# Performance work log

Hardware: AMD Instinct MI355X
Metric: run time of the kernel (lower is better)

The kernel has to match this reference:

```python
import jax, jax.numpy as jnp
import numpy as np
import math

B, T, D, DI, DFF, H = 4, 1024, 1024, 256, 4096, 16
S, N, E = 16, 256, 1024          # stat_num, token_num, exemplar_len
STAT_K, TOKEN_K = 8, 16
NEG = -1e6


def setup_inputs() -> dict:
    key = jax.random.key(0)
    ks = jax.random.split(key, 32)
    r = lambda i, shape: jax.random.normal(ks[i], shape, jnp.float32)
    w = lambda i, shape: r(i, shape) * 0.02
    return dict(
        x=r(0, (B, T, D)),
        stat_enc=r(1, (B * S, N, D)),
        exemplar_enc=r(2, (B, E, D)),
        stat_feature=r(3, (B, S, D)),
        intent_embed=r(4, (B, 1, DI)),
        Wq1=w(5, (D, D)), Wk1=w(6, (D, D)), Wv1=w(7, (D, D)), Wo1=w(8, (D, D)),
        Wq_stat=w(9, (D + DI, D)), Wq_token=w(10, (D + DI, D)),
        Wk_stat=w(11, (D, D)), Wk_token=w(12, (D, D)),
        Wv_sel=w(13, (D, D)), Wo_sel=w(14, (D, D)),
        Wq2=w(15, (D + DI, D)), Wk2=w(16, (D, D)), Wv2=w(17, (D, D)), Wo2=w(18, (D, D)),
        Wg=w(19, (2 * D, 1)),
        W1=w(20, (D, DFF)), b1=jnp.zeros((DFF,), jnp.float32),
        W2=w(21, (DFF, D)), b2=jnp.zeros((D,), jnp.float32),
        g1=jnp.ones((D,), jnp.float32), be1=jnp.zeros((D,), jnp.float32),
        g2=jnp.ones((D,), jnp.float32), be2=jnp.zeros((D,), jnp.float32),
        g3=jnp.ones((D,), jnp.float32), be3=jnp.zeros((D,), jnp.float32),
        stat_valid_len=jax.random.randint(ks[22], (B,), 1, S + 1),
        example_valid_len=jax.random.randint(ks[23], (B,), 1, E + 1),
    )


def _ln(x, g, b):
    m = x.mean(-1, keepdims=True)
    v = ((x - m) ** 2).mean(-1, keepdims=True)
    return (x - m) / jnp.sqrt(v + 1e-5) * g + b


def _mha(q, k, v, valid, Wq, Wk, Wv, Wo):
    Bq, Tq, _ = q.shape
    Sk = k.shape[1]
    sp = lambda z: z.reshape(Bq, z.shape[1], H, -1).transpose(0, 2, 1, 3)  # B,H,L,dh
    qh, kh, vh = sp(q @ Wq), sp(k @ Wk), sp(v @ Wv)
    dh = qh.shape[-1]
    sc = jnp.einsum('bhtd,bhsd->bhts', qh, kh) / math.sqrt(dh)
    vl = valid[:, None, None, None] if valid.ndim == 1 else valid[:, None, :, None]
    sc = jnp.where(jnp.arange(Sk)[None, None, None, :] < vl, sc, NEG)
    w = jax.nn.softmax(sc, axis=-1)
    out = jnp.einsum('bhts,bhsd->bhtd', w, vh).transpose(0, 2, 1, 3).reshape(Bq, Tq, -1)
    return out @ Wo


def _scatter_topk(scores, k):
    # keep top-k per row, everything else -> NEG (matches torch topk+scatter)
    shp = scores.shape
    flat = scores.reshape(-1, shp[-1])
    vals, idx = jax.lax.top_k(flat, k)
    out = jnp.full_like(flat, NEG).at[jnp.arange(flat.shape[0])[:, None], idx].set(vals)
    return out.reshape(shp)


def reference(x, stat_enc, exemplar_enc, stat_feature, intent_embed,
              Wq1, Wk1, Wv1, Wo1,
              Wq_stat, Wq_token, Wk_stat, Wk_token, Wv_sel, Wo_sel,
              Wq2, Wk2, Wv2, Wo2, Wg,
              W1, b1, W2, b2,
              g1, be1, g2, be2, g3, be3,
              stat_valid_len, example_valid_len):
    # masked self-attention (training mode -> causal valid lens)
    dec_valid = jnp.broadcast_to(jnp.arange(1, T + 1)[None, :], (B, T))
    x2 = _mha(x, x, x, dec_valid, Wq1, Wk1, Wv1, Wo1)
    y = _ln(x + x2, g1, be1)
    yi = jnp.concatenate([y, jnp.broadcast_to(intent_embed, (B, T, DI))], axis=-1)

    # selective hierarchical top-k attention
    qs = yi @ Wq_stat                      # [B,T,D]
    qt = yi @ Wq_token                     # [B,T,D]
    ks = stat_feature @ Wk_stat            # [B,S,D]
    kt = (stat_enc @ Wk_token).reshape(B, S, N, D)
    vv = (stat_enc @ Wv_sel).reshape(B, S, N, D)
    scale = math.sqrt(D)
    ssc = jnp.einsum('btd,bsd->bts', qs, ks) / scale
    ssc = jnp.where(jnp.arange(S)[None, None, :] < stat_valid_len[:, None, None], ssc, NEG)
    sw = jax.nn.softmax(_scatter_topk(ssc, min(S - 1, STAT_K)), axis=-1)   # [B,T,S]
    tsc = jnp.einsum('btd,bsnd->btsn', qt, kt) / scale                      # [B,T,S,N]
    tw = jax.nn.softmax(_scatter_topk(tsc, min(N - 1, TOKEN_K)), axis=-1)
    comb = sw[..., None] * tw                                               # [B,T,S,N]
    y2s = jnp.einsum('btsn,bsnd->btd', comb, vv) @ Wo_sel

    # exemplar cross-attention
    y2e = _mha(yi, exemplar_enc, exemplar_enc, example_valid_len, Wq2, Wk2, Wv2, Wo2)

    gate = jax.nn.sigmoid(jnp.concatenate([y2s, y2e], axis=-1) @ Wg)
    y2 = gate * y2s + (1.0 - gate) * y2e
    z = _ln(y + 2.0 * y2, g2, be2)
    ffn = jax.nn.relu(z @ W1 + b1) @ W2 + b2
    return _ln(z + ffn, g3, be3)
```

## Files before the change

kernel.cpp:

```cpp
#include <hip/hip_runtime.h>

typedef unsigned short u16;
typedef short s16x8 __attribute__((ext_vector_type(8)));
typedef u16 u16x4 __attribute__((ext_vector_type(4)));
typedef float f32x4 __attribute__((ext_vector_type(4)));

#define T_N   1024
#define NEGV  -1e6f
#define MB    (1L << 20)

__device__ __forceinline__ u16 f2bf(float f) {
    unsigned u = __float_as_uint(f);
    u += 0x7fffu + ((u >> 16) & 1u);
    return (u16)(u >> 16);
}
__device__ __forceinline__ float bf2f(u16 h) {
    return __uint_as_float(((unsigned)h) << 16);
}
__device__ __forceinline__ f32x4 mfma16(s16x8 a, s16x8 b, f32x4 c) {
    return __builtin_amdgcn_mfma_f32_16x16x32_bf16(a, b, c, 0, 0, 0);
}
__device__ __forceinline__ void gll16(const u16* g, u16* l) {
    __builtin_amdgcn_global_load_lds((const __attribute__((address_space(1))) void*)g,
                                     (__attribute__((address_space(3))) void*)l, 16, 0, 0);
}
__device__ __forceinline__ int swzf(int row) {
    return ((row >> 1) & 3) | ((row & 1) << 2);
}
__device__ __forceinline__ int swzc(int col, int row) {
    return (((col >> 3) ^ swzf(row)) << 3) | (col & 7);
}

struct P6 { const float* s[6]; u16* d[6]; };

__global__ __launch_bounds__(256) void transpose_cast_batch(P6 pp, int K, int N) {
    const float* __restrict__ src = pp.s[blockIdx.z];
    u16* __restrict__ dst = pp.d[blockIdx.z];
    __shared__ float tile[32][33];
    int nb = blockIdx.x * 32, kb = blockIdx.y * 32;
    int tx = threadIdx.x & 31, ty = threadIdx.x >> 5;
    #pragma unroll
    for (int i = 0; i < 4; i++)
        tile[ty + 8*i][tx] = src[(long)(kb + ty + 8*i) * N + nb + tx];
    __syncthreads();
    #pragma unroll
    for (int i = 0; i < 4; i++)
        dst[(long)(nb + ty + 8*i) * K + kb + tx] = f2bf(tile[tx][ty + 8*i]);
}

__global__ __launch_bounds__(256) void cast_bf16_kernel(const float* __restrict__ src,
                                                        u16* __restrict__ dst, long n) {
    long i = ((long)blockIdx.x * 256 + threadIdx.x) * 4;
    if (i >= n) return;
    float4 v = *(const float4*)(src + i);
    u16x4 o = { f2bf(v.x), f2bf(v.y), f2bf(v.z), f2bf(v.w) };
    *(u16x4*)(dst + i) = o;
}

template<typename OutT, bool RELU, bool HAS_BIAS>
__global__ __launch_bounds__(256) void gemm_bt(
    const u16* __restrict__ A, const u16* __restrict__ Bt, OutT* __restrict__ C,
    const float* __restrict__ bias, int M, int N, int K,
    int lda, int ldb, int ldc,
    int batchDivA, long sA, long sB, long sC)
{
    A  += (long)(blockIdx.z / batchDivA) * sA;
    Bt += (long)blockIdx.z * sB;
    C  += (long)blockIdx.z * sC;
    __shared__ __align__(16) u16 As[4096];
    __shared__ __align__(16) u16 Bs[4096];
    const int tid = threadIdx.x;
    const int wave = tid >> 6, lane = tid & 63;
    const int quad = lane >> 4, l16 = lane & 15;
    const int wr = (wave >> 1) * 64, wc = (wave & 1) * 64;
    const long row0 = (long)blockIdx.y * 128, col0 = (long)blockIdx.x * 128;

    f32x4 acc[4][4] = {};

    const int l4r = lane >> 2;
    const int l4c = (lane & 3) * 8;
    const int ra = wave * 32 + l4r;
    const u16* Ap0 = A + (row0 + ra) * (long)lda + l4c;
    const u16* Ap1 = Ap0 + 16L * lda;
    const u16* Bp0 = Bt + (col0 + ra) * (long)ldb + l4c;
    const u16* Bp1 = Bp0 + 16L * ldb;
    u16* AsW0 = &As[(wave * 32) * 32];
    u16* AsW1 = &As[(wave * 32 + 16) * 32];
    u16* BsW0 = &Bs[(wave * 32) * 32];
    u16* BsW1 = &Bs[(wave * 32 + 16) * 32];
    const bool aok0 = (row0 + wave * 32) < M;
    const bool aok1 = (row0 + wave * 32 + 16) < M;

    for (int k0 = 0; k0 < K; k0 += 32) {
        __syncthreads();
        if (aok0) gll16(Ap0 + k0, AsW0);
        if (aok1) gll16(Ap1 + k0, AsW1);
        gll16(Bp0 + k0, BsW0);
        gll16(Bp1 + k0, BsW1);
        __syncthreads();
        s16x8 af[4], bfr[4];
        #pragma unroll
        for (int i = 0; i < 4; i++)
            af[i]  = *(const s16x8*)&As[(wr + i*16 + l16) * 32 + quad*8];
        #pragma unroll
        for (int j = 0; j < 4; j++)
            bfr[j] = *(const s16x8*)&Bs[(wc + j*16 + l16) * 32 + quad*8];
        #pragma unroll
        for (int i = 0; i < 4; i++)
            #pragma unroll
            for (int j = 0; j < 4; j++)
                acc[i][j] = mfma16(af[i], bfr[j], acc[i][j]);
    }

    #pragma unroll
    for (int i = 0; i < 4; i++) {
        long row = row0 + wr + i*16 + quad*4;
        #pragma unroll
        for (int j = 0; j < 4; j++) {
            long col = col0 + wc + j*16 + l16;
            float bv = 0.f;
            if constexpr (HAS_BIAS) bv = bias[col];
            #pragma unroll
            for (int r = 0; r < 4; r++) {
                if (row + r < M) {
                    float v = acc[i][j][r] + bv;
                    if constexpr (RELU) v = fmaxf(v, 0.f);
                    if constexpr (sizeof(OutT) == 2) C[(row + r) * (long)ldc + col] = f2bf(v);
                    else                             C[(row + r) * (long)ldc + col] = v;
                }
            }
        }
    }
}

template<typename OutT, bool RELU, bool HAS_BIAS>
__global__ __launch_bounds__(512, 4) void gemm_bt128(
    const u16* __restrict__ A, const u16* __restrict__ Bt, OutT* __restrict__ C,
    const float* __restrict__ bias, int M, int N, int K,
    int lda, int ldb, int ldc,
    int batchDivA, long sA, long sB, long sC)
{
    int bx = blockIdx.x, by = blockIdx.y;
    {
        const int nwg = gridDim.x * gridDim.y;
        if ((nwg & 7) == 0) {
            const int flat = by * gridDim.x + bx;
            const int nf = (flat & 7) * (nwg >> 3) + (flat >> 3);
            bx = nf % gridDim.x;
            by = nf / gridDim.x;
        }
    }
    A  += (long)(blockIdx.z / batchDivA) * sA;
    Bt += (long)blockIdx.z * sB;
    C  += (long)blockIdx.z * sC;
    __shared__ __align__(16) u16 As[3][4096];
    __shared__ __align__(16) u16 Bs[3][8192];
    const int tid = threadIdx.x;
    const int wave = tid >> 6, lane = tid & 63;
    const int quad = lane >> 4, l16 = lane & 15;
    const int wm = wave >> 2, wn = wave & 3;
    const long row0 = (long)by * 128, col0 = (long)bx * 256;

    const int srow = tid >> 2;
    const int scol = ((tid & 3) ^ ((srow >> 1) & 3)) * 8;
    const u16* Ag = A  + (row0 + srow) * (long)lda + scol;
    const u16* Bg = Bt + (col0 + srow) * (long)ldb + scol;
    const int ldsoff = wave * 512;

    f32x4 acc[4][4] = {};
    const int NT = K >> 5;

    auto stage = [&](int kt, int buf) {
        gll16(Ag + (long)kt * 32,            &As[buf][ldsoff]);
        gll16(Bg + (long)kt * 32,            &Bs[buf][ldsoff]);
        gll16(Bg + (long)kt * 32 + 128L*ldb, &Bs[buf][4096 + ldsoff]);
    };

    stage(0, 0);
    if (NT > 1) {
        stage(1, 1);
        asm volatile("s_waitcnt vmcnt(3)" ::: "memory");
    } else {
        asm volatile("s_waitcnt vmcnt(0)" ::: "memory");
    }
    __builtin_amdgcn_s_barrier();
    __builtin_amdgcn_sched_barrier(0);

    const int arow = wm * 64 + l16;
    const int brow = wn * 64 + l16;
    const int kq   = (quad ^ ((l16 >> 1) & 3)) * 8;

    int slot = 0;
    for (int kt = 0; kt < NT; ++kt) {
        const u16* Ab = As[slot];
        const u16* Bb = Bs[slot];
        const int s2 = (slot + 2 >= 3) ? slot - 1 : slot + 2;

        s16x8 af[4], bfr[4];
        #pragma unroll
        for (int j = 0; j < 4; ++j)
            bfr[j] = *(const s16x8*)&Bb[(brow + j*16) * 32 + kq];
        #pragma unroll
        for (int i = 0; i < 4; ++i)
            af[i] = *(const s16x8*)&Ab[(arow + i*16) * 32 + kq];

        if (kt + 2 < NT) stage(kt + 2, s2);

        #pragma unroll
        for (int i = 0; i < 4; ++i)
            #pragma unroll
            for (int j = 0; j < 4; ++j)
                acc[i][j] = mfma16(af[i], bfr[j], acc[i][j]);

        if (kt + 2 < NT)      asm volatile("s_waitcnt vmcnt(3)" ::: "memory");
        else if (kt + 1 < NT) asm volatile("s_waitcnt vmcnt(0)" ::: "memory");
        __builtin_amdgcn_s_barrier();
        __builtin_amdgcn_sched_barrier(0);
        slot = (slot + 1 >= 3) ? 0 : slot + 1;
    }

    #pragma unroll
    for (int i = 0; i < 4; ++i) {
        const long row = row0 + wm*64 + i*16 + quad*4;
        #pragma unroll
        for (int j = 0; j < 4; ++j) {
            const long col = col0 + wn*64 + j*16 + l16;
            float bv = 0.f;
            if constexpr (HAS_BIAS) bv = bias[col];
            #pragma unroll
            for (int r = 0; r < 4; ++r) {
                float v = acc[i][j][r] + bv;
                if constexpr (RELU) v = fmaxf(v, 0.f);
                if constexpr (sizeof(OutT) == 2) C[(row + r) * (long)ldc + col] = f2bf(v);
                else                             C[(row + r) * (long)ldc + col] = v;
            }
        }
    }
}

template<bool CAUSAL>
__global__ __launch_bounds__(256, 4) void flash_attn_kernel(
    const u16* __restrict__ Q, const u16* __restrict__ Kg, const u16* __restrict__ Vg,
    const int* __restrict__ valid_len, u16* __restrict__ O,
    int qld, int kld, int vld)
{
    const int h = blockIdx.y, b = blockIdx.z;
    const int qt0 = blockIdx.x * 64;
    const int tid = threadIdx.x;
    const int wave = tid >> 6, lane = tid & 63;
    const int quad = lane >> 4, l16 = lane & 15;

    __shared__ __align__(16) u16 Ks[2][64][64];
    __shared__ __align__(16) u16 Vt[2][64][64];
    __shared__ __align__(16) u16 Ps[4][16][64];

    s16x8 aq[2];
    {
        const u16* qp = Q + ((long)b * T_N + qt0 + wave*16 + l16) * qld + h * 64 + quad * 8;
        aq[0] = *(const s16x8*)qp;
        aq[1] = *(const s16x8*)(qp + 32);
    }

    const int ksr = tid >> 2;
    const int ks2 = (tid & 3) * 2;
    const int vsr = tid & 63;
    const int vd0 = (tid >> 6) * 16;

    const u16* kp = Kg + ((long)b * T_N + ksr) * (long)kld + h * 64 + ks2 * 8;
    const u16* vp = Vg + ((long)b * T_N + vsr) * (long)vld + h * 64 + vd0;
    const long kstep = 64L * kld, vstep = 64L * vld;

    const int fl  = swzf(l16);
    const int kc0 = ((quad ^ fl) & 7) * 8;
    const int kc1 = (((quad + 4) ^ fl) & 7) * 8;

    float m_i[4] = {-1e30f, -1e30f, -1e30f, -1e30f};
    float l_i[4] = {0.f, 0.f, 0.f, 0.f};
    f32x4 o_acc[4] = {};

    int vl = 0, kend;
    if (CAUSAL) kend = qt0 + 64;
    else { vl = valid_len[b]; kend = (vl + 63) & ~63; }
    const int nt = kend >> 6;

    s16x8 krA, krB, vrA, vrB;
    krA = *(const s16x8*)kp;       krB = *(const s16x8*)(kp + 8);
    vrA = *(const s16x8*)vp;       vrB = *(const s16x8*)(vp + 8);
    kp += kstep; vp += vstep;
    {
        *(s16x8*)&Ks[0][ksr][swzc(ks2*8,     ksr)] = krA;
        *(s16x8*)&Ks[0][ksr][swzc(ks2*8 + 8, ksr)] = krB;
        #pragma unroll
        for (int j = 0; j < 8; ++j) {
            Vt[0][vd0 + j    ][swzc(vsr, vd0 + j    )] = (u16)vrA[j];
            Vt[0][vd0 + 8 + j][swzc(vsr, vd0 + 8 + j)] = (u16)vrB[j];
        }
    }
    __syncthreads();

    for (int t = 0; t < nt; ++t) {
        const int cur = t & 1;
        const bool more = (t + 1) < nt;
        if (more) {
            krA = *(const s16x8*)kp;  krB = *(const s16x8*)(kp + 8);
            vrA = *(const s16x8*)vp;  vrB = *(const s16x8*)(vp + 8);
            kp += kstep; vp += vstep;
        }
        f32x4 sc[4] = {};
        __builtin_amdgcn_s_setprio(1);
        #pragma unroll
        for (int j = 0; j < 4; ++j) {
            s16x8 bk0 = *(const s16x8*)&Ks[cur][j*16 + l16][kc0];
            sc[j] = mfma16(aq[0], bk0, sc[j]);
        }
        #pragma unroll
        for (int j = 0; j < 4; ++j) {
            s16x8 bk1 = *(const s16x8*)&Ks[cur][j*16 + l16][kc1];
            sc[j] = mfma16(aq[1], bk1, sc[j]);
        }
        __builtin_amdgcn_s_setprio(0);
        const int kv0 = t * 64;
        const int qrow = qt0 + wave*16 + quad*4;
        #pragma unroll
        for (int j = 0; j < 4; ++j) {
            int kcol = kv0 + j*16 + l16;
            #pragma unroll
            for (int r = 0; r < 4; ++r) {
                float s = sc[j][r] * 0.125f;
                bool ok = CAUSAL ? (kcol <= qrow + r) : (kcol < vl);
                sc[j][r] = ok ? s : -1e30f;
            }
        }
        float alpha[4];
        #pragma unroll
        for (int r = 0; r < 4; ++r) {
            float mx = fmaxf(fmaxf(sc[0][r], sc[1][r]), fmaxf(sc[2][r], sc[3][r]));
            #pragma unroll
            for (int d = 1; d < 16; d <<= 1) mx = fmaxf(mx, __shfl_xor(mx, d, 64));
            float mn = fmaxf(m_i[r], mx);
            alpha[r] = __expf(m_i[r] - mn);
            m_i[r] = mn;
        }
        float rsum[4] = {0.f, 0.f, 0.f, 0.f};
        #pragma unroll
        for (int j = 0; j < 4; ++j)
            #pragma unroll
            for (int r = 0; r < 4; ++r) {
                float pv = __expf(sc[j][r] - m_i[r]);
                sc[j][r] = pv;
                rsum[r] += pv;
            }
        #pragma unroll
        for (int r = 0; r < 4; ++r) {
            #pragma unroll
            for (int d = 1; d < 16; d <<= 1) rsum[r] += __shfl_xor(rsum[r], d, 64);
            l_i[r] = l_i[r] * alpha[r] + rsum[r];
        }
        #pragma unroll
        for (int j = 0; j < 4; ++j)
            #pragma unroll
            for (int r = 0; r < 4; ++r)
                Ps[wave][quad*4 + r][swzc(j*16 + l16, quad*4 + r)] = f2bf(sc[j][r]);
        #pragma unroll
        for (int j2 = 0; j2 < 4; ++j2)
            #pragma unroll
            for (int r = 0; r < 4; ++r)
                o_acc[j2][r] *= alpha[r];
        __builtin_amdgcn_s_setprio(1);
        {
            s16x8 ap0 = *(const s16x8*)&Ps[wave][l16][kc0];
            #pragma unroll
            for (int j2 = 0; j2 < 4; ++j2) {
                s16x8 bv = *(const s16x8*)&Vt[cur][j2*16 + l16][kc0];
                o_acc[j2] = mfma16(ap0, bv, o_acc[j2]);
            }
            s16x8 ap1 = *(const s16x8*)&Ps[wave][l16][kc1];
            #pragma unroll
            for (int j2 = 0; j2 < 4; ++j2) {
                s16x8 bv = *(const s16x8*)&Vt[cur][j2*16 + l16][kc1];
                o_acc[j2] = mfma16(ap1, bv, o_acc[j2]);
            }
        }
        __builtin_amdgcn_s_setprio(0);
        if (more) {
            const int nb = cur ^ 1;
            *(s16x8*)&Ks[nb][ksr][swzc(ks2*8,     ksr)] = krA;
            *(s16x8*)&Ks[nb][ksr][swzc(ks2*8 + 8, ksr)] = krB;
            #pragma unroll
            for (int j = 0; j < 8; ++j) {
                Vt[nb][vd0 + j    ][swzc(vsr, vd0 + j    )] = (u16)vrA[j];
                Vt[nb][vd0 + 8 + j][swzc(vsr, vd0 + 8 + j)] = (u16)vrB[j];
            }
        }
        __syncthreads();
    }

    #pragma unroll
    for (int j2 = 0; j2 < 4; ++j2) {
        #pragma unroll
        for (int r = 0; r < 4; ++r) {
            float v = o_acc[j2][r] / l_i[r];
            long row = (long)b * T_N + qt0 + wave*16 + quad*4 + r;
            O[row * 1024 + h*64 + j2*16 + l16] = f2bf(v);
        }
    }
}

__global__ __launch_bounds__(256) void ssc_kernel(
    const u16* __restrict__ qs, const u16* __restrict__ ks,
    const int* __restrict__ svl, float* __restrict__ ssc, int qld)
{
    const int t = blockIdx.x, b = blockIdx.y;
    const int wave = threadIdx.x >> 6, lane = threadIdx.x & 63;
    const u16* qrow = qs + ((long)b * T_N + t) * qld + lane * 16;
    const int vl = svl[b];
    for (int s = wave; s < 16; s += 4) {
        const u16* krow = ks + ((long)b * 16 + s) * 1024 + lane * 16;
        float acc = 0.f;
        #pragma unroll
        for (int seg = 0; seg < 2; seg++) {
            s16x8 qv = *(const s16x8*)(qrow + seg*8);
            s16x8 kv = *(const s16x8*)(krow + seg*8);
            #pragma unroll
            for (int j = 0; j < 8; j++) acc += bf2f((u16)qv[j]) * bf2f((u16)kv[j]);
        }
        #pragma unroll
        for (int d = 1; d < 64; d <<= 1) acc += __shfl_xor(acc, d, 64);
        if (lane == 0)
            ssc[((long)b * T_N + t) * 16 + s] = (s < vl) ? acc * (1.f/32.f) : NEGV;
    }
}

__global__ __launch_bounds__(256) void select_combine_kernel(
    const float* __restrict__ ssc, const float* __restrict__ tsc,
    const u16* __restrict__ vv, u16* __restrict__ out, int t0, int vld)
{
    const int tl = blockIdx.x, b = blockIdx.y;
    const int tg = t0 + tl;
    const int tid = threadIdx.x;
    const int wave = tid >> 6, lane = tid & 63;
    __shared__ float coeff[128];
    __shared__ long  rowoff[128];
    __shared__ int   sel_s[8];
    __shared__ float sel_w[8];

    if (wave == 0) {
        float cur = (lane < 16) ? ssc[((long)b * T_N + tg) * 16 + lane] : -3e38f;
        float mx0 = 0.f, ssum = 0.f, myv = -3e38f;
        int myi = 0;
        #pragma unroll
        for (int it = 0; it < 8; it++) {
            float mv = cur; int mi = lane;
            #pragma unroll
            for (int d = 1; d < 64; d <<= 1) {
                float ov = __shfl_xor(mv, d, 64);
                int   oi = __shfl_xor(mi, d, 64);
                if (ov > mv || (ov == mv && oi < mi)) { mv = ov; mi = oi; }
            }
            if (it == 0) mx0 = mv;
            ssum += __expf(mv - mx0);
            if (lane == it) { myv = mv; myi = mi; }
            if (lane == mi) cur = -3e38f;
        }
        if (lane < 8) { sel_s[lane] = myi; sel_w[lane] = __expf(myv - mx0) / ssum; }
    }
    __syncthreads();

    for (int slot = wave; slot < 8; slot += 4) {
        int s = sel_s[slot];
        float sw = sel_w[slot];
        const float* trow = tsc + (((long)b * 16 + s) * 512 + tl) * 256;
        float4 lv4 = *(const float4*)(trow + lane * 4);
        float loc[4] = { lv4.x, lv4.y, lv4.z, lv4.w };
        float mx0 = 0.f, tsum = 0.f, myv = -3e38f;
        int myi = 0;
        for (int it = 0; it < 16; it++) {
            float mv = -3e38f; int mi = 0;
            #pragma unroll
            for (int u = 0; u < 4; u++)
                if (loc[u] > mv) { mv = loc[u]; mi = lane*4 + u; }
            #pragma unroll
            for (int d = 1; d < 64; d <<= 1) {
                float ov = __shfl_xor(mv, d, 64);
                int   oi = __shfl_xor(mi, d, 64);
                if (ov > mv || (ov == mv && oi < mi)) { mv = ov; mi = oi; }
            }
            if (it == 0) mx0 = mv * (1.f/32.f);
            tsum += __expf(mv * (1.f/32.f) - mx0);
            if (lane == it) { myv = mv; myi = mi; }
            if ((mi >> 2) == lane) {
                int u = mi & 3;
                if (u == 0) loc[0] = -3e38f;
                else if (u == 1) loc[1] = -3e38f;
                else if (u == 2) loc[2] = -3e38f;
                else loc[3] = -3e38f;
            }
        }
        if (lane < 16) {
            coeff[slot * 16 + lane]  = sw * __expf(myv * (1.f/32.f) - mx0) / tsum;
            rowoff[slot * 16 + lane] = (long)((b * 16 + s) * 256 + myi) * vld;
        }
    }
    __syncthreads();

    const int d0 = tid * 4;
    float a0 = 0.f, a1 = 0.f, a2 = 0.f, a3 = 0.f;
    for (int r = 0; r < 128; r++) {
        float c = coeff[r];
        const u16* vp = vv + rowoff[r] + d0;
        u16x4 v4 = *(const u16x4*)vp;
        a0 += c * bf2f(v4[0]);
        a1 += c * bf2f(v4[1]);
        a2 += c * bf2f(v4[2]);
        a3 += c * bf2f(v4[3]);
    }
    u16x4 o4 = { f2bf(a0), f2bf(a1), f2bf(a2), f2bf(a3) };
    *(u16x4*)(out + ((long)b * T_N + tg) * 1024 + d0) = o4;
}

__device__ __forceinline__ float block_sum(float v, float* red) {
    #pragma unroll
    for (int d = 1; d < 64; d <<= 1) v += __shfl_xor(v, d, 64);
    __syncthreads();
    if ((threadIdx.x & 63) == 0) red[threadIdx.x >> 6] = v;
    __syncthreads();
    return red[0] + red[1] + red[2] + red[3];
}

__global__ __launch_bounds__(256) void ln1_kernel(
    const float* __restrict__ x, const float* __restrict__ x2,
    const float* __restrict__ intent, const float* __restrict__ g, const float* __restrict__ be,
    u16* __restrict__ yi)
{
    __shared__ float red[4];
    const long row = blockIdx.x;
    const int tid = threadIdx.x;
    const long base = row * 1024 + tid * 4;
    float4 xv = *(const float4*)(x + base);
    float4 dv = *(const float4*)(x2 + base);
    float h0 = xv.x + dv.x, h1 = xv.y + dv.y, h2 = xv.z + dv.z, h3 = xv.w + dv.w;
    float s1 = block_sum(h0 + h1 + h2 + h3, red);
    float s2 = block_sum(h0*h0 + h1*h1 + h2*h2 + h3*h3, red);
    float mean = s1 * (1.f/1024.f);
    float var = s2 * (1.f/1024.f) - mean * mean;
    float inv = rsqrtf(var + 1e-5f);
    const int c = tid * 4;
    float4 gv = *(const float4*)(g + c);
    float4 bv = *(const float4*)(be + c);
    float o0 = (h0 - mean) * inv * gv.x + bv.x;
    float o1 = (h1 - mean) * inv * gv.y + bv.y;
    float o2 = (h2 - mean) * inv * gv.z + bv.z;
    float o3 = (h3 - mean) * inv * gv.w + bv.w;
    u16x4 ob = { f2bf(o0), f2bf(o1), f2bf(o2), f2bf(o3) };
    *(u16x4*)(yi + row * 1280 + c) = ob;
    const int b = (int)(row >> 10);
    yi[row * 1280 + 1024 + tid] = f2bf(intent[b * 256 + tid]);
}

__global__ __launch_bounds__(256) void gate_ln2_kernel(
    const u16* __restrict__ yi, const float* __restrict__ y2s, const float* __restrict__ y2e,
    const float* __restrict__ Wg, const float* __restrict__ g, const float* __restrict__ be,
    float* __restrict__ z, u16* __restrict__ zbf)
{
    __shared__ float red[4];
    const long row = blockIdx.x;
    const int tid = threadIdx.x;
    const long base = row * 1024 + tid * 4;
    const int c = tid * 4;
    float4 sv = *(const float4*)(y2s + base);
    float4 ev = *(const float4*)(y2e + base);
    float4 w1 = *(const float4*)(Wg + c);
    float4 w2 = *(const float4*)(Wg + 1024 + c);
    float dot = sv.x*w1.x + sv.y*w1.y + sv.z*w1.z + sv.w*w1.w
              + ev.x*w2.x + ev.y*w2.y + ev.z*w2.z + ev.w*w2.w;
    float tot = block_sum(dot, red);
    float gate = 1.f / (1.f + __expf(-tot));
    u16x4 yv4 = *(const u16x4*)(yi + row * 1280 + c);
    float h0 = bf2f(yv4[0]) + 2.f * (gate * sv.x + (1.f - gate) * ev.x);
    float h1 = bf2f(yv4[1]) + 2.f * (gate * sv.y + (1.f - gate) * ev.y);
    float h2 = bf2f(yv4[2]) + 2.f * (gate * sv.z + (1.f - gate) * ev.z);
    float h3 = bf2f(yv4[3]) + 2.f * (gate * sv.w + (1.f - gate) * ev.w);
    float s1 = block_sum(h0 + h1 + h2 + h3, red);
    float s2 = block_sum(h0*h0 + h1*h1 + h2*h2 + h3*h3, red);
    float mean = s1 * (1.f/1024.f);
    float var = s2 * (1.f/1024.f) - mean * mean;
    float inv = rsqrtf(var + 1e-5f);
    float4 gv = *(const float4*)(g + c);
    float4 bv = *(const float4*)(be + c);
    float o0 = (h0 - mean) * inv * gv.x + bv.x;
    float o1 = (h1 - mean) * inv * gv.y + bv.y;
    float o2 = (h2 - mean) * inv * gv.z + bv.z;
    float o3 = (h3 - mean) * inv * gv.w + bv.w;
    *(float4*)(z + base) = make_float4(o0, o1, o2, o3);
    u16x4 ob = { f2bf(o0), f2bf(o1), f2bf(o2), f2bf(o3) };
    *(u16x4*)(zbf + row * 1024 + c) = ob;
}

__global__ __launch_bounds__(256) void ln3_kernel(
    const float* __restrict__ z, const float* __restrict__ p0, const float* __restrict__ p1,
    const float* __restrict__ b2,
    const float* __restrict__ g, const float* __restrict__ be, float* __restrict__ out)
{
    __shared__ float red[4];
    const long row = blockIdx.x;
    const int tid = threadIdx.x;
    const long base = row * 1024 + tid * 4;
    const int c = tid * 4;
    float4 zv = *(const float4*)(z + base);
    float4 f0 = *(const float4*)(p0 + base);
    float4 f1 = *(const float4*)(p1 + base);
    float4 bb = *(const float4*)(b2 + c);
    float h0 = zv.x + f0.x + f1.x + bb.x;
    float h1 = zv.y + f0.y + f1.y + bb.y;
    float h2 = zv.z + f0.z + f1.z + bb.z;
    float h3 = zv.w + f0.w + f1.w + bb.w;
    float s1 = block_sum(h0 + h1 + h2 + h3, red);
    float s2 = block_sum(h0*h0 + h1*h1 + h2*h2 + h3*h3, red);
    float mean = s1 * (1.f/1024.f);
    float var = s2 * (1.f/1024.f) - mean * mean;
    float inv = rsqrtf(var + 1e-5f);
    float4 gv = *(const float4*)(g + c);
    float4 bv = *(const float4*)(be + c);
    float o0 = (h0 - mean) * inv * gv.x + bv.x;
    float o1 = (h1 - mean) * inv * gv.y + bv.y;
    float o2 = (h2 - mean) * inv * gv.z + bv.z;
    float o3 = (h3 - mean) * inv * gv.w + bv.w;
    *(float4*)(out + base) = make_float4(o0, o1, o2, o3);
}

extern "C" void kernel_launch(void* const* d_in, const int* in_sizes, int n_in,
                              void* d_out, int out_size, void* d_ws, size_t ws_size,
                              hipStream_t stream)
{
    (void)in_sizes; (void)n_in; (void)out_size; (void)ws_size;
    const float* x      = (const float*)d_in[0];
    const float* stat_e = (const float*)d_in[1];
    const float* exem   = (const float*)d_in[2];
    const float* sfeat  = (const float*)d_in[3];
    const float* intent = (const float*)d_in[4];
    const float* Wg  = (const float*)d_in[19];
    const float* b1  = (const float*)d_in[21];
    const float* b2  = (const float*)d_in[23];
    const float* g1  = (const float*)d_in[24]; const float* be1 = (const float*)d_in[25];
    const float* g2  = (const float*)d_in[26]; const float* be2 = (const float*)d_in[27];
    const float* g3  = (const float*)d_in[28]; const float* be3 = (const float*)d_in[29];
    const int* svl = (const int*)d_in[30];
    const int* evl = (const int*)d_in[31];
    float* outp = (float*)d_out;

    char* base = (char*)d_ws;
    u16*  bufA  = (u16*)(base + 0*MB);
    u16*  qkv1  = (u16*)(base + 8*MB);
    float* x2a  = (float*)(base + 8*MB);
    u16*  kv2   = (u16*)(base + 8*MB);
    u16*  w1t   = (u16*)(base + 8*MB);
    u16*  w2t   = (u16*)(base + 16*MB);
    u16*  yibf  = (u16*)(base + 32*MB);
    u16*  buf3  = (u16*)(base + 42*MB);
    u16*  zbf   = (u16*)(base + 42*MB);
    u16*  sebf  = (u16*)(base + 66*MB);
    float* tsch = (float*)(base + 66*MB);
    u16*  hid   = (u16*)(base + 66*MB);
    u16*  ktvv  = (u16*)(base + 98*MB);
    float* y2sf = (float*)(base + 98*MB);
    float* p0f  = (float*)(base + 98*MB);
    u16*  exbf  = (u16*)(base + 114*MB);
    float* y2ef = (float*)(base + 122*MB);
    float* zf   = (float*)(base + 138*MB);
    u16*  sfbf  = (u16*)(base + 162*MB);
    u16*  ksbf  = (u16*)(base + 162*MB + 256*1024);
    float* sscf = (float*)(base + 162*MB + 512*1024);
    char* wpool = base + 163*MB;

    dim3 blk(256);
    dim3 blk512(512);
    auto cast = [&](const float* s, u16* d, long n) {
        cast_bf16_kernel<<<dim3((unsigned)((n/4 + 255) / 256)), blk, 0, stream>>>(s, d, n);
    };
    auto g_n = [&](const u16* A, const u16* Bt, u16* C, int M, int N, int K,
                   int lda, int ldb, int ldc) {
        gemm_bt<u16,false,false><<<dim3(N/128, (M+127)/128, 1), blk, 0, stream>>>(
            A, Bt, C, nullptr, M, N, K, lda, ldb, ldc, 1, 0, 0, 0);
    };
    auto g_f = [&](const u16* A, const u16* Bt, float* C, int M, int N, int K,
                   int lda, int ldb, int ldc) {
        gemm_bt<float,false,false><<<dim3(N/128, (M+127)/128, 1), blk, 0, stream>>>(
            A, Bt, C, nullptr, M, N, K, lda, ldb, ldc, 1, 0, 0, 0);
    };
    auto g128_n = [&](const u16* A, const u16* Bt, u16* C, int M, int N, int K,
                      int lda, int ldb, int ldc) {
        gemm_bt128<u16,false,false><<<dim3(N/256, M/128, 1), blk512, 0, stream>>>(
            A, Bt, C, nullptr, M, N, K, lda, ldb, ldc, 1, 0, 0, 0);
    };

    u16* wqkv1t = (u16*)wpool;
    u16* wo1t   = (u16*)(wpool) + 3L*1024*1024;
    {
        P6 pp{};
        pp.s[0]=(const float*)d_in[5]; pp.d[0]=wqkv1t;
        pp.s[1]=(const float*)d_in[6]; pp.d[1]=wqkv1t + 1L*1024*1024;
        pp.s[2]=(const float*)d_in[7]; pp.d[2]=wqkv1t + 2L*1024*1024;
        pp.s[3]=(const float*)d_in[8]; pp.d[3]=wo1t;
        transpose_cast_batch<<<dim3(32, 32, 4), blk, 0, stream>>>(pp, 1024, 1024);
    }
    cast(x, bufA, 4096L*1024);
    g128_n(bufA, wqkv1t, qkv1, 4096, 3072, 1024, 1024, 1024, 3072);
    flash_attn_kernel<true><<<dim3(16, 16, 4), blk, 0, stream>>>(
        qkv1, qkv1 + 1024, qkv1 + 2048, nullptr, bufA, 3072, 3072, 3072);
    g_f(bufA, wo1t, x2a, 4096, 1024, 1024, 1024, 1024, 1024);
    ln1_kernel<<<dim3(4096), blk, 0, stream>>>(x, x2a, intent, g1, be1, yibf);

    u16* wq3t = (u16*)wpool;
    {
        P6 pp{};
        pp.s[0]=(const float*)d_in[9];  pp.d[0]=wq3t;
        pp.s[1]=(const float*)d_in[10]; pp.d[1]=wq3t + 1L*1024*1280;
        pp.s[2]=(const float*)d_in[15]; pp.d[2]=wq3t + 2L*1024*1280;
        transpose_cast_batch<<<dim3(32, 40, 3), blk, 0, stream>>>(pp, 1280, 1024);
    }
    g128_n(yibf, wq3t, buf3, 4096, 3072, 1280, 1280, 1280, 3072);
    u16* wkst = (u16*)wpool;
    u16* wkv  = (u16*)(wpool) + 1L*1024*1024;
    {
        P6 pp{};
        pp.s[0]=(const float*)d_in[11]; pp.d[0]=wkst;
        pp.s[1]=(const float*)d_in[12]; pp.d[1]=wkv;
        pp.s[2]=(const float*)d_in[13]; pp.d[2]=wkv + 1L*1024*1024;
        transpose_cast_batch<<<dim3(32, 32, 3), blk, 0, stream>>>(pp, 1024, 1024);
    }
    cast(sfeat, sfbf, 64L*1024);
    cast(stat_e, sebf, 16384L*1024);
    g_n(sfbf, wkst, ksbf, 64, 1024, 1024, 1024, 1024, 1024);
    g128_n(sebf, wkv, ktvv, 16384, 2048, 1024, 1024, 1024, 2048);
    ssc_kernel<<<dim3(1024, 4), blk, 0, stream>>>(buf3, ksbf, svl, sscf, 3072);
    for (int hh = 0; hh < 2; hh++) {
        long t0 = hh * 512;
        gemm_bt<float,false,false><<<dim3(2, 4, 64), blk, 0, stream>>>(
            buf3 + 1024 + t0*3072, ktvv, tsch, nullptr, 512, 256, 1024,
            3072, 2048, 256, 16, (long)T_N*3072, 256L*2048, 512L*256);
        select_combine_kernel<<<dim3(512, 4), blk, 0, stream>>>(
            sscf, tsch, ktvv + 1024, bufA, (int)t0, 2048);
    }
    u16* wost = (u16*)wpool;
    u16* wkv2 = (u16*)(wpool) + 1L*1024*1024;
    u16* wo2t = (u16*)(wpool) + 3L*1024*1024;
    {
        P6 pp{};
        pp.s[0]=(const float*)d_in[14]; pp.d[0]=wost;
        pp.s[1]=(const float*)d_in[16]; pp.d[1]=wkv2;
        pp.s[2]=(const float*)d_in[17]; pp.d[2]=wkv2 + 1L*1024*1024;
        pp.s[3]=(const float*)d_in[18]; pp.d[3]=wo2t;
        transpose_cast_batch<<<dim3(32, 32, 4), blk, 0, stream>>>(pp, 1024, 1024);
    }
    g_f(bufA, wost, y2sf, 4096, 1024, 1024, 1024, 1024, 1024);

    cast(exem, exbf, 4096L*1024);
    g128_n(exbf, wkv2, kv2, 4096, 2048, 1024, 1024, 1024, 2048);
    flash_attn_kernel<false><<<dim3(16, 16, 4), blk, 0, stream>>>(
        buf3 + 2048, kv2, kv2 + 1024, evl, bufA, 3072, 2048, 2048);
    g_f(bufA, wo2t, y2ef, 4096, 1024, 1024, 1024, 1024, 1024);

    gate_ln2_kernel<<<dim3(4096), blk, 0, stream>>>(yibf, y2sf, y2ef, Wg, g2, be2, zf, zbf);

    {
        P6 pp{}; pp.s[0] = (const float*)d_in[20]; pp.d[0] = w1t;
        transpose_cast_batch<<<dim3(128, 32, 1), blk, 0, stream>>>(pp, 1024, 4096);
    }
    {
        P6 pp{}; pp.s[0] = (const float*)d_in[22]; pp.d[0] = w2t;
        transpose_cast_batch<<<dim3(32, 128, 1), blk, 0, stream>>>(pp, 4096, 1024);
    }
    gemm_bt128<u16,true,true><<<dim3(16, 32, 1), blk512, 0, stream>>>(
        zbf, w1t, hid, b1, 4096, 4096, 1024, 1024, 1024, 4096, 1, 0, 0, 0);
    gemm_bt<float,false,false><<<dim3(8, 32, 2), blk, 0, stream>>>(
        hid, w2t, p0f, nullptr, 4096, 1024, 2048, 4096, 4096, 1024,
        1, 2048, 2048, 4096L*1024);

    ln3_kernel<<<dim3(4096), blk, 0, stream>>>(zf, p0f, p0f + 4096L*1024, b2, g3, be3, outp);
}
```

Baseline: 1.001 ms.

## Restructure select-combine: redundant stat top-k per wave, paired token top-k, XCD-aware mapping

Every wave now computes the stat top-8 redundantly in registers using integer sort keys, which removes the wave-0-only phase and one block barrier. Each wave then runs two token top-16 selections interleaved in one loop to overlap shuffle latency. Block indices are remapped so each XCD works on a contiguous batch/token range for better L2 locality. The gather-accumulate uses 8-wide bf16 loads split across two thread halves with an LDS reduction. In exchange it does redundant stat-selection work, holds more registers, and relies on the hardcoded grid shape (8 XCDs, 512 tokens, 4 batches) for the index remap.

```diff
diff --git a/kernel.cpp b/kernel.cpp
--- a/kernel.cpp
+++ b/kernel.cpp
@@ -29,6 +29,10 @@
 }
 __device__ __forceinline__ int swzc(int col, int row) {
     return (((col >> 3) ^ swzf(row)) << 3) | (col & 7);
+}
+__device__ __forceinline__ unsigned fkey(float f) {
+    unsigned u = __float_as_uint(f);
+    return (u & 0x80000000u) ? ~u : (u | 0x80000000u);
 }
 
 struct P6 { const float* s[6]; u16* d[6]; };
@@ -435,87 +439,134 @@
     const float* __restrict__ ssc, const float* __restrict__ tsc,
     const u16* __restrict__ vv, u16* __restrict__ out, int t0, int vld)
 {
-    const int tl = blockIdx.x, b = blockIdx.y;
+    int tl, b;
+    {
+        const int flat = blockIdx.y * gridDim.x + blockIdx.x;
+        const int xcd = flat & 7;
+        b  = xcd >> 1;
+        tl = ((xcd & 1) << 8) + (flat >> 3);
+    }
     const int tg = t0 + tl;
     const int tid = threadIdx.x;
     const int wave = tid >> 6, lane = tid & 63;
     __shared__ float coeff[128];
-    __shared__ long  rowoff[128];
-    __shared__ int   sel_s[8];
-    __shared__ float sel_w[8];
-
-    if (wave == 0) {
-        float cur = (lane < 16) ? ssc[((long)b * T_N + tg) * 16 + lane] : -3e38f;
-        float mx0 = 0.f, ssum = 0.f, myv = -3e38f;
-        int myi = 0;
-        #pragma unroll
-        for (int it = 0; it < 8; it++) {
-            float mv = cur; int mi = lane;
+    __shared__ int   rowoff[128];
+    __shared__ float pacc[128][9];
+
+    int   ss8[8]; float sw8[8];
+    {
+        float v = (lane < 16) ? ssc[((long)b * T_N + tg) * 16 + lane] : -3e38f;
+        unsigned key = fkey(v);
+        float mx0 = 0.f, ssum = 0.f;
+        #pragma unroll
+        for (int it = 0; it < 8; ++it) {
+            unsigned k = key; int mi = lane;
             #pragma unroll
             for (int d = 1; d < 64; d <<= 1) {
-                float ov = __shfl_xor(mv, d, 64);
-                int   oi = __shfl_xor(mi, d, 64);
-                if (ov > mv || (ov == mv && oi < mi)) { mv = ov; mi = oi; }
-            }
+                unsigned ok = __shfl_xor(k, d, 64);
+                int oi = __shfl_xor(mi, d, 64);
+                if (ok > k || (ok == k && oi < mi)) { k = ok; mi = oi; }
+            }
+            float mv = __shfl(v, mi, 64);
             if (it == 0) mx0 = mv;
-            ssum += __expf(mv - mx0);
-            if (lane == it) { myv = mv; myi = mi; }
-            if (lane == mi) cur = -3e38f;
-        }
-        if (lane < 8) { sel_s[lane] = myi; sel_w[lane] = __expf(myv - mx0) / ssum; }
+            float w = __expf(mv - mx0);
+            ssum += w;
+            ss8[it] = mi; sw8[it] = w;
+            if (lane == mi) key = 0u;
+        }
+        float inv = 1.f / ssum;
+        #pragma unroll
+        for (int it = 0; it < 8; ++it) sw8[it] *= inv;
+    }
+    int sA, sB; float wA, wB;
+    if      (wave == 0) { sA = ss8[0]; sB = ss8[4]; wA = sw8[0]; wB = sw8[4]; }
+    else if (wave == 1) { sA = ss8[1]; sB = ss8[5]; wA = sw8[1]; wB = sw8[5]; }
+    else if (wave == 2) { sA = ss8[2]; sB = ss8[6]; wA = sw8[2]; wB = sw8[6]; }
+    else                { sA = ss8[3]; sB = ss8[7]; wA = sw8[3]; wB = sw8[7]; }
+
+    {
+        const float* trowA = tsc + (((long)b * 16 + sA) * 512 + tl) * 256;
+        const float* trowB = tsc + (((long)b * 16 + sB) * 512 + tl) * 256;
+        float4 a4 = *(const float4*)(trowA + lane * 4);
+        float4 b4 = *(const float4*)(trowB + lane * 4);
+        float locA[4] = { a4.x, a4.y, a4.z, a4.w };
+        float locB[4] = { b4.x, b4.y, b4.z, b4.w };
+        unsigned kA[4], kB[4];
+        #pragma unroll
+        for (int u = 0; u < 4; ++u) { kA[u] = fkey(locA[u]); kB[u] = fkey(locB[u]); }
+
+        float mxA = 0.f, mxB = 0.f, tsA = 0.f, tsB = 0.f;
+        float mywA = 0.f, mywB = 0.f;
+        int   myiA = 0, myiB = 0;
+        for (int it = 0; it < 16; ++it) {
+            unsigned ka = kA[0]; int ua = 0;
+            if (kA[1] > ka) { ka = kA[1]; ua = 1; }
+            if (kA[2] > ka) { ka = kA[2]; ua = 2; }
+            if (kA[3] > ka) { ka = kA[3]; ua = 3; }
+            unsigned kb = kB[0]; int ub = 0;
+            if (kB[1] > kb) { kb = kB[1]; ub = 1; }
+            if (kB[2] > kb) { kb = kB[2]; ub = 2; }
+            if (kB[3] > kb) { kb = kB[3]; ub = 3; }
+            int mia = lane * 4 + ua, mib = lane * 4 + ub;
+            #pragma unroll
+            for (int d = 1; d < 64; d <<= 1) {
+                unsigned oa = __shfl_xor(ka, d, 64);
+                int oia = __shfl_xor(mia, d, 64);
+                if (oa > ka || (oa == ka && oia < mia)) { ka = oa; mia = oia; }
+                unsigned ob = __shfl_xor(kb, d, 64);
+                int oib = __shfl_xor(mib, d, 64);
+                if (ob > kb || (ob == kb && oib < mib)) { kb = ob; mib = oib; }
+            }
+            int ea = mia & 3, la = mia >> 2;
+            int eb = mib & 3, lb = mib >> 2;
+            float cand_a = (ea == 0) ? locA[0] : (ea == 1) ? locA[1] : (ea == 2) ? locA[2] : locA[3];
+            float cand_b = (eb == 0) ? locB[0] : (eb == 1) ? locB[1] : (eb == 2) ? locB[2] : locB[3];
+            float mva = __shfl(cand_a, la, 64) * (1.f/32.f);
+            float mvb = __shfl(cand_b, lb, 64) * (1.f/32.f);
+            if (it == 0) { mxA = mva; mxB = mvb; }
+            float ewa = __expf(mva - mxA), ewb = __expf(mvb - mxB);
+            tsA += ewa; tsB += ewb;
+            if (lane == it) { mywA = ewa; myiA = mia; mywB = ewb; myiB = mib; }
+            if (la == lane) {
+                if (ea == 0) kA[0] = 0u; else if (ea == 1) kA[1] = 0u;
+                else if (ea == 2) kA[2] = 0u; else kA[3] = 0u;
+            }
+            if (lb == lane) {
+                if (eb == 0) kB[0] = 0u; else if (eb == 1) kB[1] = 0u;
+                else if (eb == 2) kB[2] = 0u; else kB[3] = 0u;
+            }
+        }
+        if (lane < 16) {
+            coeff[wave * 16 + lane]        = wA * mywA / tsA;
+            rowoff[wave * 16 + lane]       = ((b * 16 + sA) * 256 + myiA) * vld;
+            coeff[(wave + 4) * 16 + lane]  = wB * mywB / tsB;
+            rowoff[(wave + 4) * 16 + lane] = ((b * 16 + sB) * 256 + myiB) * vld;
+        }
     }
     __syncthreads();
 
-    for (int slot = wave; slot < 8; slot += 4) {
-        int s = sel_s[slot];
-        float sw = sel_w[slot];
-        const float* trow = tsc + (((long)b * 16 + s) * 512 + tl) * 256;
-        float4 lv4 = *(const float4*)(trow + lane * 4);
-        float loc[4] = { lv4.x, lv4.y, lv4.z, lv4.w };
-        float mx0 = 0.f, tsum = 0.f, myv = -3e38f;
-        int myi = 0;
-        for (int it = 0; it < 16; it++) {
-            float mv = -3e38f; int mi = 0;
-            #pragma unroll
-            for (int u = 0; u < 4; u++)
-                if (loc[u] > mv) { mv = loc[u]; mi = lane*4 + u; }
-            #pragma unroll
-            for (int d = 1; d < 64; d <<= 1) {
-                float ov = __shfl_xor(mv, d, 64);
-                int   oi = __shfl_xor(mi, d, 64);
-                if (ov > mv || (ov == mv && oi < mi)) { mv = ov; mi = oi; }
-            }
-            if (it == 0) mx0 = mv * (1.f/32.f);
-            tsum += __expf(mv * (1.f/32.f) - mx0);
-            if (lane == it) { myv = mv; myi = mi; }
-            if ((mi >> 2) == lane) {
-                int u = mi & 3;
-                if (u == 0) loc[0] = -3e38f;
-                else if (u == 1) loc[1] = -3e38f;
-                else if (u == 2) loc[2] = -3e38f;
-                else loc[3] = -3e38f;
-            }
-        }
-        if (lane < 16) {
-            coeff[slot * 16 + lane]  = sw * __expf(myv * (1.f/32.f) - mx0) / tsum;
-            rowoff[slot * 16 + lane] = (long)((b * 16 + s) * 256 + myi) * vld;
-        }
-    }
-    __syncthreads();
-
-    const int d0 = tid * 4;
-    float a0 = 0.f, a1 = 0.f, a2 = 0.f, a3 = 0.f;
-    for (int r = 0; r < 128; r++) {
+    const int p  = tid >> 7;
+    const int d0 = (tid & 127) * 8;
+    const int q  = tid & 127;
+    float a[8] = {};
+    for (int r = p; r < 128; r += 2) {
         float c = coeff[r];
         const u16* vp = vv + rowoff[r] + d0;
-        u16x4 v4 = *(const u16x4*)vp;
-        a0 += c * bf2f(v4[0]);
-        a1 += c * bf2f(v4[1]);
-        a2 += c * bf2f(v4[2]);
-        a3 += c * bf2f(v4[3]);
-    }
-    u16x4 o4 = { f2bf(a0), f2bf(a1), f2bf(a2), f2bf(a3) };
-    *(u16x4*)(out + ((long)b * T_N + tg) * 1024 + d0) = o4;
+        s16x8 v8 = *(const s16x8*)vp;
+        #pragma unroll
+        for (int j = 0; j < 8; ++j) a[j] += c * bf2f((u16)v8[j]);
+    }
+    if (p == 1) {
+        #pragma unroll
+        for (int j = 0; j < 8; ++j) pacc[q][j] = a[j];
+    }
+    __syncthreads();
+    if (p == 0) {
+        s16x8 ov;
+        #pragma unroll
+        for (int j = 0; j < 8; ++j) ov[j] = (short)f2bf(a[j] + pacc[q][j]);
+        *(s16x8*)&out[((long)b * T_N + tg) * 1024 + d0] = ov;
+    }
 }
 
 __device__ __forceinline__ float block_sum(float v, float* red) {
```

Result: no change. 1.006 ms (+0.4%).
